# Performance work log

Hardware: AMD Instinct MI355X
Metric: run time of the kernel (lower is better)

Reference implementation:

```python
import jax, jax.numpy as jnp
import numpy as np

B, N, E, C = 4, 131072, 8388608, 16  # batch, num_nodes, num_edges, num_classes


def setup_inputs() -> dict:
    key = jax.random.key(0)
    k1, k2, k3, k4, k5, k6 = jax.random.split(key, 6)
    nodes_feat_list = jax.random.normal(k1, (B, N, 1), dtype=jnp.float32)
    # every node must appear at least once as a source (degree assert in the module)
    src = jnp.concatenate([jnp.arange(N, dtype=jnp.int64) if False else jnp.arange(N),
                           jax.random.randint(k2, (E - N,), 0, N)])
    dst = jax.random.randint(k3, (E,), 0, N)
    edges0 = jnp.stack([src, dst], axis=0)              # (2, E)
    edges_index_list = jnp.broadcast_to(edges0[None], (B, 2, E))
    graph_label_list = jax.random.randint(k4, (B,), 0, C)
    fc_w = jax.random.normal(k5, (C, N), dtype=jnp.float32) / np.float32(np.sqrt(N))
    fc_b = jax.random.normal(k6, (C,), dtype=jnp.float32) * 0.01
    return {"nodes_feat_list": nodes_feat_list, "fc_w": fc_w, "fc_b": fc_b,
            "edges_index_list": edges_index_list, "graph_label_list": graph_label_list}


def reference(nodes_feat_list, fc_w, fc_b, edges_index_list, graph_label_list):
    # Only graph 0's edge list is used by the original module everywhere.
    src = edges_index_list[0, 0]                        # (E,) target nodes
    dst = edges_index_list[0, 1]                        # (E,) source/neighbor nodes
    n = nodes_feat_list.shape[1]
    # degree^{-1/2} per node (torch.unique(return_counts=True) == bincount here)
    deg = jnp.zeros((n,), nodes_feat_list.dtype).at[src].add(1.0)
    dscale = (deg ** -0.5)[:, None]                     # (N, 1)
    x = nodes_feat_list * dscale                        # (B, N, 1)
    xs = x[..., 0]                                      # (B, N)
    # torch scatter_add_ with index of shape (1, E) only writes batch row 0;
    # all other batch rows of the aggregation remain zero (faithful to source).
    agg0 = jnp.zeros((n,), xs.dtype).at[src].add(xs[0, dst])
    agg = jnp.zeros_like(xs).at[0].set(agg0)            # (B, N)
    y = (agg[..., None] * dscale).transpose(0, 2, 1)    # (B, 1, N)
    return jnp.einsum('bfn,cn->bfc', y, fc_w) + fc_b    # (B, 1, C)
```

## Files before the change

### kernel.cpp

```cpp
#include <hip/hip_runtime.h>

#define N_NODES   131072
#define N_EDGES   8388608
#define N_CLASSES 16
#define N_BATCH   4

#define N_SLICES        256
#define EDGES_PER_SLICE (N_EDGES / N_SLICES)
#define HIST_WORDS      (N_NODES / 4)

typedef int v4i __attribute__((ext_vector_type(4)));

__device__ __forceinline__ unsigned f2bf(float f) {
    unsigned x = __float_as_uint(f);
    return (x + 0x7FFFu + ((x >> 16) & 1u)) >> 16;
}
__device__ __forceinline__ float bf_lo(unsigned w) { return __uint_as_float(w << 16); }
__device__ __forceinline__ float bf_hi(unsigned w) { return __uint_as_float(w & 0xFFFF0000u); }


__global__ __launch_bounds__(1024)
void hist_kernel(const int* __restrict__ src, unsigned int* __restrict__ partials) {
    __shared__ unsigned int hist[HIST_WORDS];
    uint4* h4 = (uint4*)hist;
    #pragma unroll
    for (int i = threadIdx.x; i < HIST_WORDS / 4; i += 1024)
        h4[i] = make_uint4(0u, 0u, 0u, 0u);
    __syncthreads();

    const int slice = blockIdx.x;
    const v4i* s4 = (const v4i*)(src + slice * EDGES_PER_SLICE);
    #pragma unroll
    for (int i = threadIdx.x; i < EDGES_PER_SLICE / 4; i += 1024) {
        v4i v = __builtin_nontemporal_load(s4 + i);
        atomicAdd(&hist[v[0] >> 2], 1u << ((v[0] & 3) << 3));
        atomicAdd(&hist[v[1] >> 2], 1u << ((v[1] & 3) << 3));
        atomicAdd(&hist[v[2] >> 2], 1u << ((v[2] & 3) << 3));
        atomicAdd(&hist[v[3] >> 2], 1u << ((v[3] & 3) << 3));
    }
    __syncthreads();

    uint4* p4 = (uint4*)(partials + (size_t)slice * HIST_WORDS);
    #pragma unroll
    for (int i = threadIdx.x; i < HIST_WORDS / 4; i += 1024)
        p4[i] = h4[i];
}

__global__ __launch_bounds__(256)
void reduce_finalize_kernel(const unsigned int* __restrict__ partials,
                            const float* __restrict__ feat0,
                            const float* __restrict__ fc_w,
                            uint4* __restrict__ ub4,
                            float* __restrict__ xs0) {
    int t = blockIdx.x * 256 + threadIdx.x;
    unsigned d0 = 0, d1 = 0, d2 = 0, d3 = 0;
    #pragma unroll 8
    for (int s = 0; s < N_SLICES; ++s) {
        unsigned p = partials[(size_t)s * HIST_WORDS + t];
        d0 += p & 255u;
        d1 += (p >> 8) & 255u;
        d2 += (p >> 16) & 255u;
        d3 += (p >> 24);
    }
    float dsx = rsqrtf((float)d0);
    float dsy = rsqrtf((float)d1);
    float dsz = rsqrtf((float)d2);
    float dsw = rsqrtf((float)d3);

    float4 f = ((const float4*)feat0)[t];
    ((float4*)xs0)[t] = make_float4(f.x * dsx, f.y * dsy, f.z * dsz, f.w * dsw);

    float row0[16], row1[16], row2[16], row3[16];
    #pragma unroll
    for (int c = 0; c < N_CLASSES; ++c) {
        float4 w = ((const float4*)(fc_w + (size_t)c * N_NODES))[t];
        row0[c] = dsx * w.x;
        row1[c] = dsy * w.y;
        row2[c] = dsz * w.z;
        row3[c] = dsw * w.w;
    }
    size_t base = (size_t)(4 * t) * 2;
    #pragma unroll
    for (int k = 0; k < 2; ++k)
        ub4[base + k] = make_uint4(
            f2bf(row0[8*k+0]) | (f2bf(row0[8*k+1]) << 16),
            f2bf(row0[8*k+2]) | (f2bf(row0[8*k+3]) << 16),
            f2bf(row0[8*k+4]) | (f2bf(row0[8*k+5]) << 16),
            f2bf(row0[8*k+6]) | (f2bf(row0[8*k+7]) << 16));
    #pragma unroll
    for (int k = 0; k < 2; ++k)
        ub4[base + 2 + k] = make_uint4(
            f2bf(row1[8*k+0]) | (f2bf(row1[8*k+1]) << 16),
            f2bf(row1[8*k+2]) | (f2bf(row1[8*k+3]) << 16),
            f2bf(row1[8*k+4]) | (f2bf(row1[8*k+5]) << 16),
            f2bf(row1[8*k+6]) | (f2bf(row1[8*k+7]) << 16));
    #pragma unroll
    for (int k = 0; k < 2; ++k)
        ub4[base + 4 + k] = make_uint4(
            f2bf(row2[8*k+0]) | (f2bf(row2[8*k+1]) << 16),
            f2bf(row2[8*k+2]) | (f2bf(row2[8*k+3]) << 16),
            f2bf(row2[8*k+4]) | (f2bf(row2[8*k+5]) << 16),
            f2bf(row2[8*k+6]) | (f2bf(row2[8*k+7]) << 16));
    #pragma unroll
    for (int k = 0; k < 2; ++k)
        ub4[base + 6 + k] = make_uint4(
            f2bf(row3[8*k+0]) | (f2bf(row3[8*k+1]) << 16),
            f2bf(row3[8*k+2]) | (f2bf(row3[8*k+3]) << 16),
            f2bf(row3[8*k+4]) | (f2bf(row3[8*k+5]) << 16),
            f2bf(row3[8*k+6]) | (f2bf(row3[8*k+7]) << 16));
}

__global__ void out_init_kernel(const float* __restrict__ fc_b, float* __restrict__ out) {
    int t = threadIdx.x;
    if (t < N_BATCH * N_CLASSES) out[t] = fc_b[t & (N_CLASSES - 1)];
}

__global__ __launch_bounds__(256)
void gather_kernel(const int* __restrict__ src, const int* __restrict__ dst,
                   const float* __restrict__ xs0, const uint4* __restrict__ ub4,
                   float* __restrict__ out) {
    const v4i* s4 = (const v4i*)src;
    const v4i* d4 = (const v4i*)dst;

    float acc[N_CLASSES];
    #pragma unroll
    for (int c = 0; c < N_CLASSES; ++c) acc[c] = 0.0f;

    const int stride = 2048 * 256;
    int tid = blockIdx.x * 256 + threadIdx.x;

    for (int i = tid; i < N_EDGES / 4; i += stride) {
        v4i s = __builtin_nontemporal_load(s4 + i);
        v4i d = __builtin_nontemporal_load(d4 + i);

        #define EDGE(SS, DD)                                                   \
        {                                                                      \
            float x = xs0[DD];                                                 \
            size_t b = (size_t)(SS) * 2;                                       \
            uint4 r0 = ub4[b], r1 = ub4[b + 1];                                \
            acc[0]  = fmaf(bf_lo(r0.x), x, acc[0]);                            \
            acc[1]  = fmaf(bf_hi(r0.x), x, acc[1]);                            \
            acc[2]  = fmaf(bf_lo(r0.y), x, acc[2]);                            \
            acc[3]  = fmaf(bf_hi(r0.y), x, acc[3]);                            \
            acc[4]  = fmaf(bf_lo(r0.z), x, acc[4]);                            \
            acc[5]  = fmaf(bf_hi(r0.z), x, acc[5]);                            \
            acc[6]  = fmaf(bf_lo(r0.w), x, acc[6]);                            \
            acc[7]  = fmaf(bf_hi(r0.w), x, acc[7]);                            \
            acc[8]  = fmaf(bf_lo(r1.x), x, acc[8]);                            \
            acc[9]  = fmaf(bf_hi(r1.x), x, acc[9]);                            \
            acc[10] = fmaf(bf_lo(r1.y), x, acc[10]);                           \
            acc[11] = fmaf(bf_hi(r1.y), x, acc[11]);                           \
            acc[12] = fmaf(bf_lo(r1.z), x, acc[12]);                           \
            acc[13] = fmaf(bf_hi(r1.z), x, acc[13]);                           \
            acc[14] = fmaf(bf_lo(r1.w), x, acc[14]);                           \
            acc[15] = fmaf(bf_hi(r1.w), x, acc[15]);                           \
        }
        EDGE(s[0], d[0])
        EDGE(s[1], d[1])
        EDGE(s[2], d[2])
        EDGE(s[3], d[3])
        #undef EDGE
    }

    __shared__ float part[4][N_CLASSES];
    int lane = threadIdx.x & 63;
    int wid  = threadIdx.x >> 6;
    #pragma unroll
    for (int c = 0; c < N_CLASSES; ++c) {
        float v = acc[c];
        #pragma unroll
        for (int off = 32; off > 0; off >>= 1) v += __shfl_down(v, off, 64);
        if (lane == 0) part[wid][c] = v;
    }
    __syncthreads();
    if (threadIdx.x < N_CLASSES) {
        int c = threadIdx.x;
        float sum = part[0][c] + part[1][c] + part[2][c] + part[3][c];
        atomicAdd(&out[c], sum);
    }
}

__global__ void deg_kernel(const int* __restrict__ src, unsigned int* __restrict__ deg) {
    const int4* src4 = (const int4*)src;
    int stride = gridDim.x * blockDim.x;
    for (int i = blockIdx.x * blockDim.x + threadIdx.x; i < N_EDGES / 4; i += stride) {
        int4 s = src4[i];
        atomicAdd(&deg[s.x], 1u); atomicAdd(&deg[s.y], 1u);
        atomicAdd(&deg[s.z], 1u); atomicAdd(&deg[s.w], 1u);
    }
}
__global__ void scale_kernel(const float* __restrict__ feat0,
                             const unsigned int* __restrict__ deg,
                             float* __restrict__ dscale, float* __restrict__ xs0) {
    int n = blockIdx.x * blockDim.x + threadIdx.x;
    if (n < N_NODES) {
        float ds = rsqrtf((float)deg[n]);
        dscale[n] = ds;
        xs0[n] = feat0[n] * ds;
    }
}
__global__ void scatter_kernel(const int* __restrict__ src, const int* __restrict__ dst,
                               const float* __restrict__ xs0, float* __restrict__ agg0) {
    const int4* src4 = (const int4*)src;
    const int4* dst4 = (const int4*)dst;
    int stride = gridDim.x * blockDim.x;
    for (int i = blockIdx.x * blockDim.x + threadIdx.x; i < N_EDGES / 4; i += stride) {
        int4 s = src4[i]; int4 d = dst4[i];
        atomicAdd(&agg0[s.x], xs0[d.x]); atomicAdd(&agg0[s.y], xs0[d.y]);
        atomicAdd(&agg0[s.z], xs0[d.z]); atomicAdd(&agg0[s.w], xs0[d.w]);
    }
}
__global__ void dot_kernel(const float* __restrict__ agg0, const float* __restrict__ dscale,
                           const float* __restrict__ fc_w, float* __restrict__ out) {
    int n = blockIdx.x * blockDim.x + threadIdx.x;
    float y = agg0[n] * dscale[n];
    __shared__ float part[4][N_CLASSES];
    int lane = threadIdx.x & 63, wid = threadIdx.x >> 6;
    #pragma unroll
    for (int c = 0; c < N_CLASSES; ++c) {
        float v = y * fc_w[c * N_NODES + n];
        #pragma unroll
        for (int off = 32; off > 0; off >>= 1) v += __shfl_down(v, off, 64);
        if (lane == 0) part[wid][c] = v;
    }
    __syncthreads();
    if (threadIdx.x < N_CLASSES) {
        int c = threadIdx.x;
        atomicAdd(&out[c], part[0][c] + part[1][c] + part[2][c] + part[3][c]);
    }
}

extern "C" void kernel_launch(void* const* d_in, const int* in_sizes, int n_in,
                              void* d_out, int out_size, void* d_ws, size_t ws_size,
                              hipStream_t stream) {
    const float* nodes_feat = (const float*)d_in[0];
    const float* fc_w       = (const float*)d_in[1];
    const float* fc_b       = (const float*)d_in[2];
    const int*   edges      = (const int*)d_in[3];

    const int* src = edges;
    const int* dst = edges + N_EDGES;
    float* out = (float*)d_out;

    const size_t PARTIALS_WORDS = (size_t)N_SLICES * HIST_WORDS;
    const size_t U_WORDS        = (size_t)N_NODES * 8;
    const size_t NEED = (PARTIALS_WORDS + U_WORDS + N_NODES) * 4;

    if (ws_size >= NEED) {
        unsigned int* partials = (unsigned int*)d_ws;
        uint4* ub4 = (uint4*)((unsigned int*)d_ws + PARTIALS_WORDS);
        float* xs0 = (float*)((unsigned int*)d_ws + PARTIALS_WORDS + U_WORDS);

        hist_kernel<<<N_SLICES, 1024, 0, stream>>>(src, partials);
        reduce_finalize_kernel<<<N_NODES / 4 / 256, 256, 0, stream>>>(
            partials, nodes_feat, fc_w, ub4, xs0);
        out_init_kernel<<<1, 64, 0, stream>>>(fc_b, out);
        gather_kernel<<<2048, 256, 0, stream>>>(src, dst, xs0, ub4, out);
    } else {
        unsigned int* deg = (unsigned int*)d_ws;
        float* dscale = (float*)d_ws + N_NODES;
        float* xs0    = (float*)d_ws + 2 * N_NODES;
        float* agg0   = (float*)d_ws + 3 * N_NODES;
        hipMemsetAsync(deg, 0, N_NODES * sizeof(unsigned int), stream);
        hipMemsetAsync(agg0, 0, N_NODES * sizeof(float), stream);
        deg_kernel<<<2048, 256, 0, stream>>>(src, deg);
        scale_kernel<<<N_NODES / 256, 256, 0, stream>>>(nodes_feat, deg, dscale, xs0);
        scatter_kernel<<<2048, 256, 0, stream>>>(src, dst, xs0, agg0);
        out_init_kernel<<<1, 64, 0, stream>>>(fc_b, out);
        dot_kernel<<<N_NODES / 256, 256, 0, stream>>>(agg0, dscale, fc_w, out);
    }
}
```

Measured before the change: 129.2 us.

## Partition edges by source-node range before gathering classifier rows

```diff
diff --git a/kernel.cpp b/kernel.cpp
--- a/kernel.cpp
+++ b/kernel.cpp
@@ -9,6 +9,13 @@
 #define EDGES_PER_SLICE (N_EDGES / N_SLICES)
 #define HIST_WORDS      (N_NODES / 4)
 
+#define N_RANGES        4
+#define P1_BLOCKS       1024
+#define P1_THREADS      256
+#define N_WAVES         (P1_BLOCKS * P1_THREADS / 64)
+#define EDGES_PER_WAVE  (N_EDGES / N_WAVES)
+#define P1_ITERS        (N_EDGES / (P1_BLOCKS * P1_THREADS))
+
 typedef int v4i __attribute__((ext_vector_type(4)));
 
 __device__ __forceinline__ unsigned f2bf(float f) {
@@ -17,7 +24,6 @@
 }
 __device__ __forceinline__ float bf_lo(unsigned w) { return __uint_as_float(w << 16); }
 __device__ __forceinline__ float bf_hi(unsigned w) { return __uint_as_float(w & 0xFFFF0000u); }
-
 
 __global__ __launch_bounds__(1024)
 void hist_kernel(const int* __restrict__ src, unsigned int* __restrict__ partials) {
@@ -116,23 +122,142 @@
 }
 
 __global__ __launch_bounds__(256)
+void partition_kernel(const int* __restrict__ src, const int* __restrict__ dst,
+                      const float* __restrict__ xs0,
+                      unsigned int* __restrict__ bucket,
+                      unsigned int* __restrict__ counts) {
+    int tid  = blockIdx.x * P1_THREADS + threadIdx.x;
+    int lane = threadIdx.x & 63;
+    int gwid = tid >> 6;
+    unsigned long long lt = (1ull << lane) - 1ull;
+
+    unsigned cur0 = 0, cur1 = 0, cur2 = 0, cur3 = 0;
+    size_t b0 = ((size_t)0 * N_WAVES + gwid) * EDGES_PER_WAVE;
+    size_t b1 = ((size_t)1 * N_WAVES + gwid) * EDGES_PER_WAVE;
+    size_t b2 = ((size_t)2 * N_WAVES + gwid) * EDGES_PER_WAVE;
+    size_t b3 = ((size_t)3 * N_WAVES + gwid) * EDGES_PER_WAVE;
+
+    const int stride = P1_BLOCKS * P1_THREADS;
+    #pragma unroll 4
+    for (int k = 0; k < P1_ITERS; ++k) {
+        int i = tid + k * stride;
+        int s = __builtin_nontemporal_load(src + i);
+        int d = __builtin_nontemporal_load(dst + i);
+        float x = xs0[d];
+        unsigned rec = (unsigned)(s & 0x7FFF) | (f2bf(x) << 16);
+        int r = s >> 15;
+
+        #pragma unroll
+        for (int R = 0; R < N_RANGES; ++R) {
+            unsigned long long m = __ballot(r == R);
+            unsigned base = (R == 0) ? cur0 : (R == 1) ? cur1 : (R == 2) ? cur2 : cur3;
+            if (r == R) {
+                size_t reg = (R == 0) ? b0 : (R == 1) ? b1 : (R == 2) ? b2 : b3;
+                bucket[reg + base + __popcll(m & lt)] = rec;
+            }
+            unsigned c = (unsigned)__popcll(m);
+            if (R == 0) cur0 += c; else if (R == 1) cur1 += c;
+            else if (R == 2) cur2 += c; else cur3 += c;
+        }
+    }
+    if (lane == 0) {
+        counts[0 * N_WAVES + gwid] = cur0;
+        counts[1 * N_WAVES + gwid] = cur1;
+        counts[2 * N_WAVES + gwid] = cur2;
+        counts[3 * N_WAVES + gwid] = cur3;
+    }
+}
+
+__global__ __launch_bounds__(256)
+void gather2_kernel(const unsigned int* __restrict__ bucket,
+                    const unsigned int* __restrict__ counts,
+                    const uint4* __restrict__ ub4,
+                    float* __restrict__ out) {
+    int r    = blockIdx.x & 3;
+    int j    = blockIdx.x >> 2;
+    int w    = threadIdx.x >> 6;
+    int lane = threadIdx.x & 63;
+    int gwid = j * 4 + w;
+    size_t slot = (size_t)r * N_WAVES + gwid;
+
+    unsigned len = counts[slot];
+    const unsigned int* rec = bucket + slot * EDGES_PER_WAVE;
+    unsigned rbase = (unsigned)r << 15;
+
+    float acc[N_CLASSES];
+    #pragma unroll
+    for (int c = 0; c < N_CLASSES; ++c) acc[c] = 0.0f;
+
+    #define ACCUM(A, B, X)                                                \
+        acc[0]  = fmaf(bf_lo((A).x), (X), acc[0]);                        \
+        acc[1]  = fmaf(bf_hi((A).x), (X), acc[1]);                        \
+        acc[2]  = fmaf(bf_lo((A).y), (X), acc[2]);                        \
+        acc[3]  = fmaf(bf_hi((A).y), (X), acc[3]);                        \
+        acc[4]  = fmaf(bf_lo((A).z), (X), acc[4]);                        \
+        acc[5]  = fmaf(bf_hi((A).z), (X), acc[5]);                        \
+        acc[6]  = fmaf(bf_lo((A).w), (X), acc[6]);                        \
+        acc[7]  = fmaf(bf_hi((A).w), (X), acc[7]);                        \
+        acc[8]  = fmaf(bf_lo((B).x), (X), acc[8]);                        \
+        acc[9]  = fmaf(bf_hi((B).x), (X), acc[9]);                        \
+        acc[10] = fmaf(bf_lo((B).y), (X), acc[10]);                       \
+        acc[11] = fmaf(bf_hi((B).y), (X), acc[11]);                       \
+        acc[12] = fmaf(bf_lo((B).z), (X), acc[12]);                       \
+        acc[13] = fmaf(bf_hi((B).z), (X), acc[13]);                       \
+        acc[14] = fmaf(bf_lo((B).w), (X), acc[14]);                       \
+        acc[15] = fmaf(bf_hi((B).w), (X), acc[15]);
+
+    unsigned i = lane;
+    for (; i + 64 < len; i += 128) {
+        unsigned rc0 = __builtin_nontemporal_load(rec + i);
+        unsigned rc1 = __builtin_nontemporal_load(rec + i + 64);
+        unsigned n0 = rbase | (rc0 & 0x7FFFu);
+        unsigned n1 = rbase | (rc1 & 0x7FFFu);
+        float x0 = __uint_as_float(rc0 & 0xFFFF0000u);
+        float x1 = __uint_as_float(rc1 & 0xFFFF0000u);
+        uint4 A0 = ub4[(size_t)n0 * 2], B0 = ub4[(size_t)n0 * 2 + 1];
+        uint4 A1 = ub4[(size_t)n1 * 2], B1 = ub4[(size_t)n1 * 2 + 1];
+        ACCUM(A0, B0, x0)
+        ACCUM(A1, B1, x1)
+    }
+    for (; i < len; i += 64) {
+        unsigned rc = __builtin_nontemporal_load(rec + i);
+        unsigned n = rbase | (rc & 0x7FFFu);
+        float x = __uint_as_float(rc & 0xFFFF0000u);
+        uint4 A = ub4[(size_t)n * 2], B = ub4[(size_t)n * 2 + 1];
+        ACCUM(A, B, x)
+    }
+    #undef ACCUM
+
+    __shared__ float part[4][N_CLASSES];
+    #pragma unroll
+    for (int c = 0; c < N_CLASSES; ++c) {
+        float v = acc[c];
+        #pragma unroll
+        for (int off = 32; off > 0; off >>= 1) v += __shfl_down(v, off, 64);
+        if (lane == 0) part[w][c] = v;
+    }
+    __syncthreads();
+    if (threadIdx.x < N_CLASSES) {
+        int c = threadIdx.x;
+        float sum = part[0][c] + part[1][c] + part[2][c] + part[3][c];
+        atomicAdd(&out[c], sum);
+    }
+}
+
+__global__ __launch_bounds__(256)
 void gather_kernel(const int* __restrict__ src, const int* __restrict__ dst,
                    const float* __restrict__ xs0, const uint4* __restrict__ ub4,
                    float* __restrict__ out) {
     const v4i* s4 = (const v4i*)src;
     const v4i* d4 = (const v4i*)dst;
-
     float acc[N_CLASSES];
     #pragma unroll
     for (int c = 0; c < N_CLASSES; ++c) acc[c] = 0.0f;
-
     const int stride = 2048 * 256;
     int tid = blockIdx.x * 256 + threadIdx.x;
-
     for (int i = tid; i < N_EDGES / 4; i += stride) {
         v4i s = __builtin_nontemporal_load(s4 + i);
         v4i d = __builtin_nontemporal_load(d4 + i);
-
         #define EDGE(SS, DD)                                                   \
         {                                                                      \
             float x = xs0[DD];                                                 \
@@ -155,16 +280,11 @@
             acc[14] = fmaf(bf_lo(r1.w), x, acc[14]);                           \
             acc[15] = fmaf(bf_hi(r1.w), x, acc[15]);                           \
         }
-        EDGE(s[0], d[0])
-        EDGE(s[1], d[1])
-        EDGE(s[2], d[2])
-        EDGE(s[3], d[3])
+        EDGE(s[0], d[0]) EDGE(s[1], d[1]) EDGE(s[2], d[2]) EDGE(s[3], d[3])
         #undef EDGE
     }
-
     __shared__ float part[4][N_CLASSES];
-    int lane = threadIdx.x & 63;
-    int wid  = threadIdx.x >> 6;
+    int lane = threadIdx.x & 63, wid = threadIdx.x >> 6;
     #pragma unroll
     for (int c = 0; c < N_CLASSES; ++c) {
         float v = acc[c];
@@ -175,8 +295,7 @@
     __syncthreads();
     if (threadIdx.x < N_CLASSES) {
         int c = threadIdx.x;
-        float sum = part[0][c] + part[1][c] + part[2][c] + part[3][c];
-        atomicAdd(&out[c], sum);
+        atomicAdd(&out[c], part[0][c] + part[1][c] + part[2][c] + part[3][c]);
     }
 }
 
@@ -244,13 +363,29 @@
 
     const size_t PARTIALS_WORDS = (size_t)N_SLICES * HIST_WORDS;
     const size_t U_WORDS        = (size_t)N_NODES * 8;
-    const size_t NEED = (PARTIALS_WORDS + U_WORDS + N_NODES) * 4;
-
-    if (ws_size >= NEED) {
-        unsigned int* partials = (unsigned int*)d_ws;
-        uint4* ub4 = (uint4*)((unsigned int*)d_ws + PARTIALS_WORDS);
-        float* xs0 = (float*)((unsigned int*)d_ws + PARTIALS_WORDS + U_WORDS);
-
+    const size_t XS0_WORDS      = N_NODES;
+    const size_t COUNT_WORDS    = (size_t)N_RANGES * N_WAVES;
+    const size_t BUCKET_WORDS   = (size_t)N_RANGES * N_WAVES * EDGES_PER_WAVE;
+    const size_t NEED_FAST = (PARTIALS_WORDS + U_WORDS + XS0_WORDS) * 4;
+    const size_t NEED_BIG  = NEED_FAST + (COUNT_WORDS + BUCKET_WORDS) * 4;
+
+    unsigned int* wsw      = (unsigned int*)d_ws;
+    unsigned int* partials = wsw;
+    uint4*        ub4      = (uint4*)(wsw + PARTIALS_WORDS);
+    float*        xs0      = (float*)(wsw + PARTIALS_WORDS + U_WORDS);
+    unsigned int* counts   = wsw + PARTIALS_WORDS + U_WORDS + XS0_WORDS;
+    unsigned int* bucket   = counts + COUNT_WORDS;
+
+    if (ws_size >= NEED_BIG) {
+        hist_kernel<<<N_SLICES, 1024, 0, stream>>>(src, partials);
+        reduce_finalize_kernel<<<N_NODES / 4 / 256, 256, 0, stream>>>(
+            partials, nodes_feat, fc_w, ub4, xs0);
+        out_init_kernel<<<1, 64, 0, stream>>>(fc_b, out);
+        partition_kernel<<<P1_BLOCKS, P1_THREADS, 0, stream>>>(
+            src, dst, xs0, bucket, counts);
+        gather2_kernel<<<N_RANGES * N_WAVES / 4, 256, 0, stream>>>(
+            bucket, counts, ub4, out);
+    } else if (ws_size >= NEED_FAST) {
         hist_kernel<<<N_SLICES, 1024, 0, stream>>>(src, partials);
         reduce_finalize_kernel<<<N_NODES / 4 / 256, 256, 0, stream>>>(
             partials, nodes_feat, fc_w, ub4, xs0);
@@ -259,13 +394,13 @@
     } else {
         unsigned int* deg = (unsigned int*)d_ws;
         float* dscale = (float*)d_ws + N_NODES;
-        float* xs0    = (float*)d_ws + 2 * N_NODES;
+        float* xs0b   = (float*)d_ws + 2 * N_NODES;
         float* agg0   = (float*)d_ws + 3 * N_NODES;
         hipMemsetAsync(deg, 0, N_NODES * sizeof(unsigned int), stream);
         hipMemsetAsync(agg0, 0, N_NODES * sizeof(float), stream);
         deg_kernel<<<2048, 256, 0, stream>>>(src, deg);
-        scale_kernel<<<N_NODES / 256, 256, 0, stream>>>(nodes_feat, deg, dscale, xs0);
-        scatter_kernel<<<2048, 256, 0, stream>>>(src, dst, xs0, agg0);
+        scale_kernel<<<N_NODES / 256, 256, 0, stream>>>(nodes_feat, deg, dscale, xs0b);
+        scatter_kernel<<<2048, 256, 0, stream>>>(src, dst, xs0b, agg0);
         out_init_kernel<<<1, 64, 0, stream>>>(fc_b, out);
         dot_kernel<<<N_NODES / 256, 256, 0, stream>>>(agg0, dscale, fc_w, out);
     }
```

New measurement: 155.6 us. 1.2x slower.

## Partition edges by source-node range so gather reads fc rows from LDS

Applied to the files above, without the earlier changes.

```diff
diff --git a/kernel.cpp b/kernel.cpp
--- a/kernel.cpp
+++ b/kernel.cpp
@@ -9,6 +9,12 @@
 #define EDGES_PER_SLICE (N_EDGES / N_SLICES)
 #define HIST_WORDS      (N_NODES / 4)
 
+#define RANGE_BITS      12
+#define NODES_PER_RANGE 4096
+#define N_RANGES2       (N_NODES / NODES_PER_RANGE)
+#define TILE            4096
+#define N_TILES         (N_EDGES / TILE)
+
 typedef int v4i __attribute__((ext_vector_type(4)));
 
 __device__ __forceinline__ unsigned f2bf(float f) {
@@ -17,7 +23,6 @@
 }
 __device__ __forceinline__ float bf_lo(unsigned w) { return __uint_as_float(w << 16); }
 __device__ __forceinline__ float bf_hi(unsigned w) { return __uint_as_float(w & 0xFFFF0000u); }
-
 
 __global__ __launch_bounds__(1024)
 void hist_kernel(const int* __restrict__ src, unsigned int* __restrict__ partials) {
@@ -51,7 +56,8 @@
                             const float* __restrict__ feat0,
                             const float* __restrict__ fc_w,
                             uint4* __restrict__ ub4,
-                            float* __restrict__ xs0) {
+                            float* __restrict__ xs0,
+                            unsigned int* __restrict__ range_cnt) {
     int t = blockIdx.x * 256 + threadIdx.x;
     unsigned d0 = 0, d1 = 0, d2 = 0, d3 = 0;
     #pragma unroll 8
@@ -62,6 +68,12 @@
         d2 += (p >> 16) & 255u;
         d3 += (p >> 24);
     }
+
+    unsigned tot = d0 + d1 + d2 + d3;
+    #pragma unroll
+    for (int off = 32; off > 0; off >>= 1) tot += __shfl_down(tot, off, 64);
+    if ((threadIdx.x & 63) == 0) atomicAdd(&range_cnt[t >> 10], tot);
+
     float dsx = rsqrtf((float)d0);
     float dsy = rsqrtf((float)d1);
     float dsz = rsqrtf((float)d2);
@@ -110,9 +122,152 @@
             f2bf(row3[8*k+6]) | (f2bf(row3[8*k+7]) << 16));
 }
 
+__global__ void prefix_kernel(const unsigned int* __restrict__ range_cnt,
+                              unsigned int* __restrict__ base,
+                              unsigned int* __restrict__ cursor) {
+    if (threadIdx.x == 0) {
+        unsigned acc = 0;
+        for (int r = 0; r < N_RANGES2; ++r) {
+            base[r] = acc; cursor[r] = acc; acc += range_cnt[r];
+        }
+        base[N_RANGES2] = acc;
+    }
+}
+
 __global__ void out_init_kernel(const float* __restrict__ fc_b, float* __restrict__ out) {
     int t = threadIdx.x;
     if (t < N_BATCH * N_CLASSES) out[t] = fc_b[t & (N_CLASSES - 1)];
+}
+
+__global__ __launch_bounds__(256)
+void scatter_part_kernel(const int* __restrict__ src, const int* __restrict__ dst,
+                         unsigned int* __restrict__ bucket,
+                         unsigned int* __restrict__ cursor) {
+    __shared__ unsigned cnt[N_RANGES2];
+    __shared__ unsigned pfx[N_RANGES2];
+    __shared__ unsigned gbase[N_RANGES2];
+    __shared__ unsigned place[N_RANGES2];
+    __shared__ unsigned recs[TILE];
+
+    const int tb = blockIdx.x * TILE;
+    if (threadIdx.x < N_RANGES2) cnt[threadIdx.x] = 0;
+    __syncthreads();
+
+    int s[16], d[16];
+    #pragma unroll
+    for (int k = 0; k < 16; ++k) {
+        int i = tb + threadIdx.x + k * 256;
+        s[k] = __builtin_nontemporal_load(src + i);
+        d[k] = __builtin_nontemporal_load(dst + i);
+        atomicAdd(&cnt[s[k] >> RANGE_BITS], 1u);
+    }
+    __syncthreads();
+
+    if (threadIdx.x < N_RANGES2) {
+        unsigned p = 0;
+        for (int q = 0; q < (int)threadIdx.x; ++q) p += cnt[q];
+        pfx[threadIdx.x]   = p;
+        place[threadIdx.x] = p;
+        gbase[threadIdx.x] = atomicAdd(&cursor[threadIdx.x], cnt[threadIdx.x]);
+    }
+    __syncthreads();
+
+    #pragma unroll
+    for (int k = 0; k < 16; ++k) {
+        int r = s[k] >> RANGE_BITS;
+        unsigned rec = (unsigned)(s[k] & (NODES_PER_RANGE - 1)) | ((unsigned)d[k] << RANGE_BITS);
+        unsigned slot = atomicAdd(&place[r], 1u);
+        recs[slot] = rec;
+    }
+    __syncthreads();
+
+    for (int r = 0; r < N_RANGES2; ++r) {
+        unsigned c = cnt[r], p = pfx[r], g = gbase[r];
+        for (unsigned j = threadIdx.x; j < c; j += 256)
+            bucket[(size_t)g + j] = recs[p + j];
+    }
+}
+
+__global__ __launch_bounds__(1024)
+void gather3_kernel(const unsigned int* __restrict__ bucket,
+                    const unsigned int* __restrict__ base,
+                    const float* __restrict__ xs0,
+                    const uint4* __restrict__ ub4,
+                    float* __restrict__ out) {
+    __shared__ uint4 uslice[2 * NODES_PER_RANGE];
+    __shared__ float part[16][N_CLASSES];
+
+    const int r = blockIdx.x & (N_RANGES2 - 1);
+    const int g = blockIdx.x >> 5;
+
+    const uint4* usrc = ub4 + (size_t)r * NODES_PER_RANGE * 2;
+    for (int i = threadIdx.x; i < 2 * NODES_PER_RANGE; i += 1024) {
+        uint4 v = usrc[i];
+        uslice[(i & 1) * NODES_PER_RANGE + (i >> 1)] = v;
+    }
+    __syncthreads();
+
+    const unsigned lo = base[r], hi = base[r + 1];
+
+    float acc[N_CLASSES];
+    #pragma unroll
+    for (int c = 0; c < N_CLASSES; ++c) acc[c] = 0.0f;
+
+    #define ACCUM(A, B, X)                                                \
+        acc[0]  = fmaf(bf_lo((A).x), (X), acc[0]);                        \
+        acc[1]  = fmaf(bf_hi((A).x), (X), acc[1]);                        \
+        acc[2]  = fmaf(bf_lo((A).y), (X), acc[2]);                        \
+        acc[3]  = fmaf(bf_hi((A).y), (X), acc[3]);                        \
+        acc[4]  = fmaf(bf_lo((A).z), (X), acc[4]);                        \
+        acc[5]  = fmaf(bf_hi((A).z), (X), acc[5]);                        \
+        acc[6]  = fmaf(bf_lo((A).w), (X), acc[6]);                        \
+        acc[7]  = fmaf(bf_hi((A).w), (X), acc[7]);                        \
+        acc[8]  = fmaf(bf_lo((B).x), (X), acc[8]);                        \
+        acc[9]  = fmaf(bf_hi((B).x), (X), acc[9]);                        \
+        acc[10] = fmaf(bf_lo((B).y), (X), acc[10]);                       \
+        acc[11] = fmaf(bf_hi((B).y), (X), acc[11]);                       \
+        acc[12] = fmaf(bf_lo((B).z), (X), acc[12]);                       \
+        acc[13] = fmaf(bf_hi((B).z), (X), acc[13]);                       \
+        acc[14] = fmaf(bf_lo((B).w), (X), acc[14]);                       \
+        acc[15] = fmaf(bf_hi((B).w), (X), acc[15]);
+
+    unsigned i = lo + g * 1024 + threadIdx.x;
+    for (; i + 8192 < hi; i += 16384) {
+        unsigned rc0 = __builtin_nontemporal_load(bucket + i);
+        unsigned rc1 = __builtin_nontemporal_load(bucket + i + 8192);
+        unsigned n0 = rc0 & (NODES_PER_RANGE - 1), n1 = rc1 & (NODES_PER_RANGE - 1);
+        float x0 = xs0[rc0 >> RANGE_BITS];
+        float x1 = xs0[rc1 >> RANGE_BITS];
+        uint4 A0 = uslice[n0], B0 = uslice[NODES_PER_RANGE + n0];
+        uint4 A1 = uslice[n1], B1 = uslice[NODES_PER_RANGE + n1];
+        ACCUM(A0, B0, x0)
+        ACCUM(A1, B1, x1)
+    }
+    for (; i < hi; i += 8192) {
+        unsigned rc = __builtin_nontemporal_load(bucket + i);
+        unsigned n = rc & (NODES_PER_RANGE - 1);
+        float x = xs0[rc >> RANGE_BITS];
+        uint4 A = uslice[n], B = uslice[NODES_PER_RANGE + n];
+        ACCUM(A, B, x)
+    }
+    #undef ACCUM
+
+    int lane = threadIdx.x & 63, wid = threadIdx.x >> 6;
+    #pragma unroll
+    for (int c = 0; c < N_CLASSES; ++c) {
+        float v = acc[c];
+        #pragma unroll
+        for (int off = 32; off > 0; off >>= 1) v += __shfl_down(v, off, 64);
+        if (lane == 0) part[wid][c] = v;
+    }
+    __syncthreads();
+    if (threadIdx.x < N_CLASSES) {
+        int c = threadIdx.x;
+        float sum = 0.0f;
+        #pragma unroll
+        for (int w = 0; w < 16; ++w) sum += part[w][c];
+        atomicAdd(&out[c], sum);
+    }
 }
 
 __global__ __launch_bounds__(256)
@@ -121,18 +276,14 @@
                    float* __restrict__ out) {
     const v4i* s4 = (const v4i*)src;
     const v4i* d4 = (const v4i*)dst;
-
     float acc[N_CLASSES];
     #pragma unroll
     for (int c = 0; c < N_CLASSES; ++c) acc[c] = 0.0f;
-
     const int stride = 2048 * 256;
     int tid = blockIdx.x * 256 + threadIdx.x;
-
     for (int i = tid; i < N_EDGES / 4; i += stride) {
         v4i s = __builtin_nontemporal_load(s4 + i);
         v4i d = __builtin_nontemporal_load(d4 + i);
-
         #define EDGE(SS, DD)                                                   \
         {                                                                      \
             float x = xs0[DD];                                                 \
@@ -155,16 +306,11 @@
             acc[14] = fmaf(bf_lo(r1.w), x, acc[14]);                           \
             acc[15] = fmaf(bf_hi(r1.w), x, acc[15]);                           \
         }
-        EDGE(s[0], d[0])
-        EDGE(s[1], d[1])
-        EDGE(s[2], d[2])
-        EDGE(s[3], d[3])
+        EDGE(s[0], d[0]) EDGE(s[1], d[1]) EDGE(s[2], d[2]) EDGE(s[3], d[3])
         #undef EDGE
     }
-
     __shared__ float part[4][N_CLASSES];
-    int lane = threadIdx.x & 63;
-    int wid  = threadIdx.x >> 6;
+    int lane = threadIdx.x & 63, wid = threadIdx.x >> 6;
     #pragma unroll
     for (int c = 0; c < N_CLASSES; ++c) {
         float v = acc[c];
@@ -175,8 +321,7 @@
     __syncthreads();
     if (threadIdx.x < N_CLASSES) {
         int c = threadIdx.x;
-        float sum = part[0][c] + part[1][c] + part[2][c] + part[3][c];
-        atomicAdd(&out[c], sum);
+        atomicAdd(&out[c], part[0][c] + part[1][c] + part[2][c] + part[3][c]);
     }
 }
 
@@ -244,28 +389,48 @@
 
     const size_t PARTIALS_WORDS = (size_t)N_SLICES * HIST_WORDS;
     const size_t U_WORDS        = (size_t)N_NODES * 8;
-    const size_t NEED = (PARTIALS_WORDS + U_WORDS + N_NODES) * 4;
-
-    if (ws_size >= NEED) {
-        unsigned int* partials = (unsigned int*)d_ws;
-        uint4* ub4 = (uint4*)((unsigned int*)d_ws + PARTIALS_WORDS);
-        float* xs0 = (float*)((unsigned int*)d_ws + PARTIALS_WORDS + U_WORDS);
-
+    const size_t XS0_WORDS      = N_NODES;
+    const size_t CTRL_WORDS     = 128;
+    const size_t BUCKET_WORDS   = N_EDGES;
+    const size_t NEED_FAST = (PARTIALS_WORDS + U_WORDS + XS0_WORDS) * 4;
+    const size_t NEED_PART = NEED_FAST + (CTRL_WORDS + BUCKET_WORDS) * 4;
+
+    unsigned int* wsw       = (unsigned int*)d_ws;
+    unsigned int* partials  = wsw;
+    uint4*        ub4       = (uint4*)(wsw + PARTIALS_WORDS);
+    float*        xs0       = (float*)(wsw + PARTIALS_WORDS + U_WORDS);
+    unsigned int* ctrl      = wsw + PARTIALS_WORDS + U_WORDS + XS0_WORDS;
+    unsigned int* range_cnt = ctrl;
+    unsigned int* base      = ctrl + 32;
+    unsigned int* cursor    = ctrl + 65;
+    unsigned int* bucket    = ctrl + CTRL_WORDS;
+
+    if (ws_size >= NEED_PART) {
+        hipMemsetAsync(range_cnt, 0, 32 * sizeof(unsigned int), stream);
         hist_kernel<<<N_SLICES, 1024, 0, stream>>>(src, partials);
         reduce_finalize_kernel<<<N_NODES / 4 / 256, 256, 0, stream>>>(
-            partials, nodes_feat, fc_w, ub4, xs0);
+            partials, nodes_feat, fc_w, ub4, xs0, range_cnt);
+        prefix_kernel<<<1, 64, 0, stream>>>(range_cnt, base, cursor);
+        scatter_part_kernel<<<N_TILES, 256, 0, stream>>>(src, dst, bucket, cursor);
+        out_init_kernel<<<1, 64, 0, stream>>>(fc_b, out);
+        gather3_kernel<<<N_RANGES2 * 8, 1024, 0, stream>>>(bucket, base, xs0, ub4, out);
+    } else if (ws_size >= NEED_FAST) {
+        hipMemsetAsync(ctrl, 0, 32 * sizeof(unsigned int), stream);
+        hist_kernel<<<N_SLICES, 1024, 0, stream>>>(src, partials);
+        reduce_finalize_kernel<<<N_NODES / 4 / 256, 256, 0, stream>>>(
+            partials, nodes_feat, fc_w, ub4, xs0, ctrl);
         out_init_kernel<<<1, 64, 0, stream>>>(fc_b, out);
         gather_kernel<<<2048, 256, 0, stream>>>(src, dst, xs0, ub4, out);
     } else {
         unsigned int* deg = (unsigned int*)d_ws;
         float* dscale = (float*)d_ws + N_NODES;
-        float* xs0    = (float*)d_ws + 2 * N_NODES;
+        float* xs0b   = (float*)d_ws + 2 * N_NODES;
         float* agg0   = (float*)d_ws + 3 * N_NODES;
         hipMemsetAsync(deg, 0, N_NODES * sizeof(unsigned int), stream);
         hipMemsetAsync(agg0, 0, N_NODES * sizeof(float), stream);
         deg_kernel<<<2048, 256, 0, stream>>>(src, deg);
-        scale_kernel<<<N_NODES / 256, 256, 0, stream>>>(nodes_feat, deg, dscale, xs0);
-        scatter_kernel<<<2048, 256, 0, stream>>>(src, dst, xs0, agg0);
+        scale_kernel<<<N_NODES / 256, 256, 0, stream>>>(nodes_feat, deg, dscale, xs0b);
+        scatter_kernel<<<2048, 256, 0, stream>>>(src, dst, xs0b, agg0);
         out_init_kernel<<<1, 64, 0, stream>>>(fc_b, out);
         dot_kernel<<<N_NODES / 256, 256, 0, stream>>>(agg0, dscale, fc_w, out);
     }
```

Result: slower. 138.3 us (+7.0%).

## Split gather work across thread pairs, each handling half the class row

Applied to the files above, without the earlier changes.

```diff
diff --git a/kernel.cpp b/kernel.cpp
--- a/kernel.cpp
+++ b/kernel.cpp
@@ -17,7 +17,6 @@
 }
 __device__ __forceinline__ float bf_lo(unsigned w) { return __uint_as_float(w << 16); }
 __device__ __forceinline__ float bf_hi(unsigned w) { return __uint_as_float(w & 0xFFFF0000u); }
-
 
 __global__ __launch_bounds__(1024)
 void hist_kernel(const int* __restrict__ src, unsigned int* __restrict__ partials) {
@@ -115,68 +114,76 @@
     if (t < N_BATCH * N_CLASSES) out[t] = fc_b[t & (N_CLASSES - 1)];
 }
 
-__global__ __launch_bounds__(256)
-void gather_kernel(const int* __restrict__ src, const int* __restrict__ dst,
-                   const float* __restrict__ xs0, const uint4* __restrict__ ub4,
-                   float* __restrict__ out) {
-    const v4i* s4 = (const v4i*)src;
-    const v4i* d4 = (const v4i*)dst;
-
-    float acc[N_CLASSES];
-    #pragma unroll
-    for (int c = 0; c < N_CLASSES; ++c) acc[c] = 0.0f;
-
-    const int stride = 2048 * 256;
-    int tid = blockIdx.x * 256 + threadIdx.x;
-
-    for (int i = tid; i < N_EDGES / 4; i += stride) {
-        v4i s = __builtin_nontemporal_load(s4 + i);
-        v4i d = __builtin_nontemporal_load(d4 + i);
-
-        #define EDGE(SS, DD)                                                   \
-        {                                                                      \
-            float x = xs0[DD];                                                 \
-            size_t b = (size_t)(SS) * 2;                                       \
-            uint4 r0 = ub4[b], r1 = ub4[b + 1];                                \
-            acc[0]  = fmaf(bf_lo(r0.x), x, acc[0]);                            \
-            acc[1]  = fmaf(bf_hi(r0.x), x, acc[1]);                            \
-            acc[2]  = fmaf(bf_lo(r0.y), x, acc[2]);                            \
-            acc[3]  = fmaf(bf_hi(r0.y), x, acc[3]);                            \
-            acc[4]  = fmaf(bf_lo(r0.z), x, acc[4]);                            \
-            acc[5]  = fmaf(bf_hi(r0.z), x, acc[5]);                            \
-            acc[6]  = fmaf(bf_lo(r0.w), x, acc[6]);                            \
-            acc[7]  = fmaf(bf_hi(r0.w), x, acc[7]);                            \
-            acc[8]  = fmaf(bf_lo(r1.x), x, acc[8]);                            \
-            acc[9]  = fmaf(bf_hi(r1.x), x, acc[9]);                            \
-            acc[10] = fmaf(bf_lo(r1.y), x, acc[10]);                           \
-            acc[11] = fmaf(bf_hi(r1.y), x, acc[11]);                           \
-            acc[12] = fmaf(bf_lo(r1.z), x, acc[12]);                           \
-            acc[13] = fmaf(bf_hi(r1.z), x, acc[13]);                           \
-            acc[14] = fmaf(bf_lo(r1.w), x, acc[14]);                           \
-            acc[15] = fmaf(bf_hi(r1.w), x, acc[15]);                           \
-        }
-        EDGE(s[0], d[0])
-        EDGE(s[1], d[1])
-        EDGE(s[2], d[2])
-        EDGE(s[3], d[3])
-        #undef EDGE
-    }
-
-    __shared__ float part[4][N_CLASSES];
+#define G_BLOCKS  2048
+#define G_THREADS 256
+#define N_PAIRS   (G_BLOCKS * G_THREADS / 2)
+#define EDGES_PER_PAIR (N_EDGES / N_PAIRS)
+
+__global__ __launch_bounds__(G_THREADS)
+void gather_pair_kernel(const int* __restrict__ src, const int* __restrict__ dst,
+                        const float* __restrict__ xs0, const uint4* __restrict__ ub4,
+                        float* __restrict__ out) {
+    const int tid  = blockIdx.x * G_THREADS + threadIdx.x;
+    const int pair = tid >> 1;
+    const int half = tid & 1;
+
+    float acc[8];
+    #pragma unroll
+    for (int c = 0; c < 8; ++c) acc[c] = 0.0f;
+
+    #define ACC8(H, X)                                   \
+        acc[0] = fmaf(bf_lo((H).x), (X), acc[0]);        \
+        acc[1] = fmaf(bf_hi((H).x), (X), acc[1]);        \
+        acc[2] = fmaf(bf_lo((H).y), (X), acc[2]);        \
+        acc[3] = fmaf(bf_hi((H).y), (X), acc[3]);        \
+        acc[4] = fmaf(bf_lo((H).z), (X), acc[4]);        \
+        acc[5] = fmaf(bf_hi((H).z), (X), acc[5]);        \
+        acc[6] = fmaf(bf_lo((H).w), (X), acc[6]);        \
+        acc[7] = fmaf(bf_hi((H).w), (X), acc[7]);
+
+    #pragma unroll 1
+    for (int k = 0; k < EDGES_PER_PAIR; k += 4) {
+        int e0 = pair + (k + 0) * N_PAIRS;
+        int e1 = pair + (k + 1) * N_PAIRS;
+        int e2 = pair + (k + 2) * N_PAIRS;
+        int e3 = pair + (k + 3) * N_PAIRS;
+        int s0 = __builtin_nontemporal_load(src + e0);
+        int d0 = __builtin_nontemporal_load(dst + e0);
+        int s1 = __builtin_nontemporal_load(src + e1);
+        int d1 = __builtin_nontemporal_load(dst + e1);
+        int s2 = __builtin_nontemporal_load(src + e2);
+        int d2 = __builtin_nontemporal_load(dst + e2);
+        int s3 = __builtin_nontemporal_load(src + e3);
+        int d3 = __builtin_nontemporal_load(dst + e3);
+
+        float x0 = xs0[d0], x1 = xs0[d1], x2 = xs0[d2], x3 = xs0[d3];
+        uint4 h0 = ub4[(size_t)s0 * 2 + half];
+        uint4 h1 = ub4[(size_t)s1 * 2 + half];
+        uint4 h2 = ub4[(size_t)s2 * 2 + half];
+        uint4 h3 = ub4[(size_t)s3 * 2 + half];
+
+        ACC8(h0, x0)
+        ACC8(h1, x1)
+        ACC8(h2, x2)
+        ACC8(h3, x3)
+    }
+    #undef ACC8
+
+    __shared__ float part[4][2][8];
     int lane = threadIdx.x & 63;
     int wid  = threadIdx.x >> 6;
     #pragma unroll
-    for (int c = 0; c < N_CLASSES; ++c) {
+    for (int c = 0; c < 8; ++c) {
         float v = acc[c];
         #pragma unroll
-        for (int off = 32; off > 0; off >>= 1) v += __shfl_down(v, off, 64);
-        if (lane == 0) part[wid][c] = v;
+        for (int off = 2; off <= 32; off <<= 1) v += __shfl_down(v, off, 64);
+        if (lane < 2) part[wid][lane][c] = v;
     }
     __syncthreads();
     if (threadIdx.x < N_CLASSES) {
-        int c = threadIdx.x;
-        float sum = part[0][c] + part[1][c] + part[2][c] + part[3][c];
-        atomicAdd(&out[c], sum);
+        int h = threadIdx.x >> 3, c = threadIdx.x & 7;
+        float sum = part[0][h][c] + part[1][h][c] + part[2][h][c] + part[3][h][c];
+        atomicAdd(&out[h * 8 + c], sum);
     }
 }
 
@@ -244,9 +251,9 @@
 
     const size_t PARTIALS_WORDS = (size_t)N_SLICES * HIST_WORDS;
     const size_t U_WORDS        = (size_t)N_NODES * 8;
-    const size_t NEED = (PARTIALS_WORDS + U_WORDS + N_NODES) * 4;
-
-    if (ws_size >= NEED) {
+    const size_t NEED_FAST = (PARTIALS_WORDS + U_WORDS + N_NODES) * 4;
+
+    if (ws_size >= NEED_FAST) {
         unsigned int* partials = (unsigned int*)d_ws;
         uint4* ub4 = (uint4*)((unsigned int*)d_ws + PARTIALS_WORDS);
         float* xs0 = (float*)((unsigned int*)d_ws + PARTIALS_WORDS + U_WORDS);
@@ -255,17 +262,17 @@
         reduce_finalize_kernel<<<N_NODES / 4 / 256, 256, 0, stream>>>(
             partials, nodes_feat, fc_w, ub4, xs0);
         out_init_kernel<<<1, 64, 0, stream>>>(fc_b, out);
-        gather_kernel<<<2048, 256, 0, stream>>>(src, dst, xs0, ub4, out);
+        gather_pair_kernel<<<G_BLOCKS, G_THREADS, 0, stream>>>(src, dst, xs0, ub4, out);
     } else {
         unsigned int* deg = (unsigned int*)d_ws;
         float* dscale = (float*)d_ws + N_NODES;
-        float* xs0    = (float*)d_ws + 2 * N_NODES;
+        float* xs0b   = (float*)d_ws + 2 * N_NODES;
         float* agg0   = (float*)d_ws + 3 * N_NODES;
         hipMemsetAsync(deg, 0, N_NODES * sizeof(unsigned int), stream);
         hipMemsetAsync(agg0, 0, N_NODES * sizeof(float), stream);
         deg_kernel<<<2048, 256, 0, stream>>>(src, deg);
-        scale_kernel<<<N_NODES / 256, 256, 0, stream>>>(nodes_feat, deg, dscale, xs0);
-        scatter_kernel<<<2048, 256, 0, stream>>>(src, dst, xs0, agg0);
+        scale_kernel<<<N_NODES / 256, 256, 0, stream>>>(nodes_feat, deg, dscale, xs0b);
+        scatter_kernel<<<2048, 256, 0, stream>>>(src, dst, xs0b, agg0);
         out_init_kernel<<<1, 64, 0, stream>>>(fc_b, out);
         dot_kernel<<<N_NODES / 256, 256, 0, stream>>>(agg0, dscale, fc_w, out);
     }
```

Measured after the change: 137.2 us. +6.2%, slower.
